# Kernel optimization log

Measured on AMD Instinct MI355X. Metric: run time of the kernel, lower is better.

Reference implementation:

```python
import jax, jax.numpy as jnp
import numpy as np
import math

B, S, H, NH = 2, 2048, 2048, 16
HD = H // NH
BASE = 10000.0


def _rope_tables():
    inv_freq = 1.0 / (BASE ** (np.arange(0, HD, 2, dtype=np.float32) / HD))
    t = np.arange(S, dtype=np.float32)
    freqs = np.einsum('i,j->ij', t, inv_freq)          # [S, HD/2]
    emb = np.concatenate([freqs, freqs], axis=-1)       # [S, HD]
    return jnp.asarray(np.cos(emb)), jnp.asarray(np.sin(emb))


def setup_inputs() -> dict:
    key = jax.random.key(0)
    ks = jax.random.split(key, 6)
    scale = 1.0 / math.sqrt(H)
    cos, sin = _rope_tables()
    causal = np.triu(np.full((S, S), -1e9, dtype=np.float32), k=1)
    attn_bias = jnp.broadcast_to(jnp.asarray(causal)[None, None], (B, 1, S, S))
    return {
        'hidden_states': jax.random.normal(ks[0], (B, S, H), jnp.float32),
        'masks': jnp.zeros((B, S, S), jnp.float32),
        'attn_bias': attn_bias,
        'cos': cos,
        'sin': sin,
        'wq': jax.random.normal(ks[1], (H, H), jnp.float32) * scale,
        'wk': jax.random.normal(ks[2], (H, H), jnp.float32) * scale,
        'wv': jax.random.normal(ks[3], (H, H), jnp.float32) * scale,
        'wo': jax.random.normal(ks[4], (H, H), jnp.float32) * scale,
        'position_ids': jnp.broadcast_to(jnp.arange(S, dtype=jnp.int64)[None], (B, S)),
    }


def _rotate_half(x):
    x1, x2 = x[..., : x.shape[-1] // 2], x[..., x.shape[-1] // 2:]
    return jnp.concatenate([-x2, x1], axis=-1)


def reference(hidden_states, masks, attn_bias, cos, sin, wq, wk, wv, wo, position_ids):
    b, s, h = hidden_states.shape
    nh, hd = NH, HD
    # QKV projections (torch Linear: x @ W.T), split heads -> [b, nh, s, hd]
    def proj(w):
        return (hidden_states @ w.T).reshape(b, s, nh, hd).transpose(0, 2, 1, 3)
    q, k, v = proj(wq), proj(wk), proj(wv)
    # RoPE
    cos_p = cos[position_ids][:, None]  # [b, 1, s, hd]
    sin_p = sin[position_ids][:, None]
    q = q * cos_p + _rotate_half(q) * sin_p
    k = k * cos_p + _rotate_half(k) * sin_p
    # attention scores with additive masks (mx_attn branch, fp math)
    att = jnp.einsum('bhqd,bhkd->bhqk', q / math.sqrt(hd), k)
    att = att + attn_bias + masks[:, None]
    att = jax.nn.softmax(att, axis=-1)
    out = jnp.einsum('bhqk,bhkd->bhqd', att, v)
    out = out.transpose(0, 2, 1, 3).reshape(b, s, h)
    return out @ wo.T
```

## Files before the change

### kernel.cpp

```cpp
#include <hip/hip_runtime.h>
#include <stdint.h>

#define B_  2
#define S_  2048
#define H_  2048
#define NH_ 16
#define HD_ 128

typedef __bf16 v8bf __attribute__((ext_vector_type(8)));
typedef float  v4f  __attribute__((ext_vector_type(4)));

__device__ __forceinline__ float b2f(unsigned short u) {
  union { unsigned int i; float f; } x; x.i = ((unsigned int)u) << 16; return x.f;
}
__device__ __forceinline__ unsigned short f2b(float f) {
  union { float f; unsigned int i; } x; x.f = f;
  unsigned int r = x.i + 0x7FFFu + ((x.i >> 16) & 1u);
  return (unsigned short)(r >> 16);
}

__device__ __forceinline__ void async16(const void* g, void* l) {
  __builtin_amdgcn_global_load_lds(
      (const __attribute__((address_space(1))) void*)g,
      (__attribute__((address_space(3))) void*)l, 16, 0, 0);
}

__global__ __launch_bounds__(256) void cvt_all(const float* __restrict__ hid,
                                               const float* __restrict__ wq,
                                               const float* __restrict__ wk,
                                               const float* __restrict__ wv,
                                               const float* __restrict__ wo,
                                               unsigned short* __restrict__ Xb,
                                               unsigned short* __restrict__ Wqb,
                                               unsigned short* __restrict__ Wkb,
                                               unsigned short* __restrict__ Wvb,
                                               unsigned short* __restrict__ Wob) {
  int bid = blockIdx.x;
  const float* src;
  unsigned short* dst;
  int rel;
  if (bid < 8192)       { src = hid; dst = Xb;  rel = bid; }
  else if (bid < 12288) { src = wq;  dst = Wqb; rel = bid - 8192; }
  else if (bid < 16384) { src = wk;  dst = Wkb; rel = bid - 12288; }
  else if (bid < 20480) { src = wv;  dst = Wvb; rel = bid - 16384; }
  else                  { src = wo;  dst = Wob; rel = bid - 20480; }
  int i = rel * 256 + threadIdx.x;
  float4 f = *(const float4*)(src + (size_t)i * 4);
  ushort4 u;
  u.x = f2b(f.x); u.y = f2b(f.y); u.z = f2b(f.z); u.w = f2b(f.w);
  *(ushort4*)(dst + (size_t)i * 4) = u;
}

__device__ __forceinline__ void gemm_tile_nt(const unsigned short* __restrict__ A,
                                             const unsigned short* __restrict__ Bm,
                                             int m0, int n0, int Kdim,
                                             unsigned short* As, unsigned short* Bs,
                                             v4f (&acc)[2][8]) {
  const int tid = threadIdx.x;
  const int lane = tid & 63, w = tid >> 6;
  const int lr = lane & 15, lg = lane >> 4;
  const int wm = w * 32;

  for (int k0 = 0; k0 < Kdim; k0 += 32) {
    __syncthreads();
#pragma unroll
    for (int i = 0; i < 2; ++i) {
      const int cbase = i * 256 + w * 64;
      const int cc = cbase + lane;
      const int row = cc >> 2, col = (cc & 3) << 3;
      async16(A  + (size_t)(m0 + row) * Kdim + k0 + col, (char*)As + (size_t)cbase * 16);
      async16(Bm + (size_t)(n0 + row) * Kdim + k0 + col, (char*)Bs + (size_t)cbase * 16);
    }
    __syncthreads();
    v8bf a[2], bb[8];
#pragma unroll
    for (int i = 0; i < 2; i++) a[i]  = *(const v8bf*)(As + (wm + i * 16 + lr) * 32 + lg * 8);
#pragma unroll
    for (int i = 0; i < 8; i++) bb[i] = *(const v8bf*)(Bs + (i * 16 + lr) * 32 + lg * 8);
#pragma unroll
    for (int mi = 0; mi < 2; mi++)
#pragma unroll
      for (int ni = 0; ni < 8; ni++)
        acc[mi][ni] = __builtin_amdgcn_mfma_f32_16x16x32_bf16(a[mi], bb[ni], acc[mi][ni], 0, 0, 0);
  }
}

__global__ __launch_bounds__(512, 2) void gemm_qkv(const unsigned short* __restrict__ X,
                                                   const unsigned short* __restrict__ Wq,
                                                   const unsigned short* __restrict__ Wk,
                                                   const unsigned short* __restrict__ Wv,
                                                   const float* __restrict__ cosT,
                                                   const float* __restrict__ sinT,
                                                   unsigned short* __restrict__ Qo,
                                                   unsigned short* __restrict__ Ko,
                                                   unsigned short* __restrict__ Vt) {
  __shared__ __align__(16) unsigned short lds[4][256 * 64];

  const int tid = threadIdx.x, lane = tid & 63, w = tid >> 6;
  const int lr = lane & 15, lg = lane >> 4;
  const int m0 = blockIdx.x * 256;
  const int by = blockIdx.y;
  const int xsw = (lr & 7) << 3;

  auto stgA = [&](const unsigned short* G, int g0, int k0, unsigned short* dst) {
#pragma unroll
    for (int i = 0; i < 4; ++i) {
      const int cbase = i * 512 + w * 64;
      const int cc = cbase + lane;
      const int row = cc >> 3;
      const int kq = (cc & 7) ^ (row & 7);
      async16(G + (size_t)(g0 + row) * H_ + k0 + kq * 8, (char*)dst + (size_t)cbase * 16);
    }
  };
  auto stgB128 = [&](const unsigned short* G, int g0, int k0, unsigned short* dst) {
#pragma unroll
    for (int i = 0; i < 2; ++i) {
      const int cbase = i * 512 + w * 64;
      const int cc = cbase + lane;
      const int row = cc >> 3;
      const int kq = (cc & 7) ^ (row & 7);
      async16(G + (size_t)(g0 + row) * H_ + k0 + kq * 8, (char*)dst + (size_t)cbase * 16);
    }
  };

  {
    const int nq = by & 7;
    const int n0 = nq * 256;
    const unsigned short* Bw = (by < 8) ? Wq : Wk;
    const int wm = w >> 1, wn = w & 1;

    v4f acc[4][8];
#pragma unroll
    for (int i = 0; i < 4; i++)
#pragma unroll
      for (int j = 0; j < 8; j++) { v4f z = {0.f, 0.f, 0.f, 0.f}; acc[i][j] = z; }

    stgA(X,  m0, 0, lds[0]);
    stgA(Bw, n0, 0, lds[1]);
    __syncthreads();

    for (int t = 0; t < 32; ++t) {
      const unsigned short* As = lds[(t & 1) * 2];
      const unsigned short* Bs = lds[(t & 1) * 2 + 1];
      unsigned short* Ad = lds[((t + 1) & 1) * 2];
      unsigned short* Bd = lds[((t + 1) & 1) * 2 + 1];
      const int kn = (t + 1) * 64;
      v8bf bf[8][2], af[2];

      if (t < 31) stgA(X, m0, kn, Ad);
#pragma unroll
      for (int ni = 0; ni < 8; ni++) {
        const unsigned short* rp = Bs + (size_t)(wn * 128 + ni * 16 + lr) * 64;
        bf[ni][0] = *(const v8bf*)(rp + ((lg * 8) ^ xsw));
        bf[ni][1] = *(const v8bf*)(rp + ((32 + lg * 8) ^ xsw));
      }
      {
        const unsigned short* rp = As + (size_t)(wm * 64 + lr) * 64;
        af[0] = *(const v8bf*)(rp + ((lg * 8) ^ xsw));
        af[1] = *(const v8bf*)(rp + ((32 + lg * 8) ^ xsw));
      }
      __builtin_amdgcn_s_barrier();
      asm volatile("s_waitcnt lgkmcnt(0)" ::: "memory");
      __builtin_amdgcn_sched_barrier(0);
      __builtin_amdgcn_s_setprio(1);
#pragma unroll
      for (int ni = 0; ni < 8; ni++) {
        acc[0][ni] = __builtin_amdgcn_mfma_f32_16x16x32_bf16(af[0], bf[ni][0], acc[0][ni], 0, 0, 0);
        acc[0][ni] = __builtin_amdgcn_mfma_f32_16x16x32_bf16(af[1], bf[ni][1], acc[0][ni], 0, 0, 0);
      }
      __builtin_amdgcn_s_setprio(0);
      __builtin_amdgcn_s_barrier();

      if (t < 31) stgA(Bw, n0, kn, Bd);
      {
        const unsigned short* rp = As + (size_t)(wm * 64 + 16 + lr) * 64;
        af[0] = *(const v8bf*)(rp + ((lg * 8) ^ xsw));
        af[1] = *(const v8bf*)(rp + ((32 + lg * 8) ^ xsw));
      }
      __builtin_amdgcn_s_barrier();
      asm volatile("s_waitcnt lgkmcnt(0)" ::: "memory");
      __builtin_amdgcn_sched_barrier(0);
      __builtin_amdgcn_s_setprio(1);
#pragma unroll
      for (int ni = 0; ni < 8; ni++) {
        acc[1][ni] = __builtin_amdgcn_mfma_f32_16x16x32_bf16(af[0], bf[ni][0], acc[1][ni], 0, 0, 0);
        acc[1][ni] = __builtin_amdgcn_mfma_f32_16x16x32_bf16(af[1], bf[ni][1], acc[1][ni], 0, 0, 0);
      }
      __builtin_amdgcn_s_setprio(0);
      __builtin_amdgcn_s_barrier();

      {
        const unsigned short* rp = As + (size_t)(wm * 64 + 32 + lr) * 64;
        af[0] = *(const v8bf*)(rp + ((lg * 8) ^ xsw));
        af[1] = *(const v8bf*)(rp + ((32 + lg * 8) ^ xsw));
      }
      __builtin_amdgcn_s_barrier();
      asm volatile("s_waitcnt lgkmcnt(0)" ::: "memory");
      __builtin_amdgcn_sched_barrier(0);
      __builtin_amdgcn_s_setprio(1);
#pragma unroll
      for (int ni = 0; ni < 8; ni++) {
        acc[2][ni] = __builtin_amdgcn_mfma_f32_16x16x32_bf16(af[0], bf[ni][0], acc[2][ni], 0, 0, 0);
        acc[2][ni] = __builtin_amdgcn_mfma_f32_16x16x32_bf16(af[1], bf[ni][1], acc[2][ni], 0, 0, 0);
      }
      __builtin_amdgcn_s_setprio(0);
      __builtin_amdgcn_s_barrier();

      {
        const unsigned short* rp = As + (size_t)(wm * 64 + 48 + lr) * 64;
        af[0] = *(const v8bf*)(rp + ((lg * 8) ^ xsw));
        af[1] = *(const v8bf*)(rp + ((32 + lg * 8) ^ xsw));
      }
      __builtin_amdgcn_s_barrier();
      asm volatile("s_waitcnt lgkmcnt(0)" ::: "memory");
      __builtin_amdgcn_sched_barrier(0);
      __builtin_amdgcn_s_setprio(1);
#pragma unroll
      for (int ni = 0; ni < 8; ni++) {
        acc[3][ni] = __builtin_amdgcn_mfma_f32_16x16x32_bf16(af[0], bf[ni][0], acc[3][ni], 0, 0, 0);
        acc[3][ni] = __builtin_amdgcn_mfma_f32_16x16x32_bf16(af[1], bf[ni][1], acc[3][ni], 0, 0, 0);
      }
      __builtin_amdgcn_s_setprio(0);
      __syncthreads();
    }

    const int h = nq * 2 + wn;
    const int rb0 = m0 + wm * 64;
    unsigned short* Out = (by < 8) ? Qo : Ko;
    const float sc = (by < 8) ? (float)(0.08838834764831845 * 1.4426950408889634) : 1.0f;
#pragma unroll
    for (int mi = 0; mi < 4; mi++)
#pragma unroll
      for (int ni = 0; ni < 4; ni++)
#pragma unroll
        for (int r = 0; r < 4; r++) {
          int row = rb0 + mi * 16 + lg * 4 + r;
          int s = row & 2047;
          int d = ni * 16 + lr;
          float c  = cosT[(size_t)s * HD_ + d];
          float sn = sinT[(size_t)s * HD_ + d];
          float x1 = acc[mi][ni][r], x2 = acc[mi][ni + 4][r];
          Out[(size_t)row * H_ + h * HD_ + d]      = f2b((x1 * c - x2 * sn) * sc);
          Out[(size_t)row * H_ + h * HD_ + d + 64] = f2b((x2 * c + x1 * sn) * sc);
        }
  }

  {
    const int n0v = by * 128;
    const int wm = w >> 1, wn = w & 1;

    v4f acc[4][4];
#pragma unroll
    for (int i = 0; i < 4; i++)
#pragma unroll
      for (int j = 0; j < 4; j++) { v4f z = {0.f, 0.f, 0.f, 0.f}; acc[i][j] = z; }

    stgA(X, m0, 0, lds[0]);
    stgB128(Wv, n0v, 0, lds[1]);
    __syncthreads();

    for (int t = 0; t < 32; ++t) {
      const unsigned short* As = lds[(t & 1) * 2];
      const unsigned short* Bs = lds[(t & 1) * 2 + 1];
      unsigned short* Ad = lds[((t + 1) & 1) * 2];
      unsigned short* Bd = lds[((t + 1) & 1) * 2 + 1];
      const int kn = (t + 1) * 64;
      v8bf bf[4][2], af[2];

      if (t < 31) stgA(X, m0, kn, Ad);
#pragma unroll
      for (int ni = 0; ni < 4; ni++) {
        const unsigned short* rp = Bs + (size_t)(wn * 64 + ni * 16 + lr) * 64;
        bf[ni][0] = *(const v8bf*)(rp + ((lg * 8) ^ xsw));
        bf[ni][1] = *(const v8bf*)(rp + ((32 + lg * 8) ^ xsw));
      }
      {
        const unsigned short* rp = As + (size_t)(wm * 64 + lr) * 64;
        af[0] = *(const v8bf*)(rp + ((lg * 8) ^ xsw));
        af[1] = *(const v8bf*)(rp + ((32 + lg * 8) ^ xsw));
      }
      __builtin_amdgcn_s_barrier();
      asm volatile("s_waitcnt lgkmcnt(0)" ::: "memory");
      __builtin_amdgcn_sched_barrier(0);
      __builtin_amdgcn_s_setprio(1);
#pragma unroll
      for (int ni = 0; ni < 4; ni++) {
        acc[0][ni] = __builtin_amdgcn_mfma_f32_16x16x32_bf16(af[0], bf[ni][0], acc[0][ni], 0, 0, 0);
        acc[0][ni] = __builtin_amdgcn_mfma_f32_16x16x32_bf16(af[1], bf[ni][1], acc[0][ni], 0, 0, 0);
      }
      __builtin_amdgcn_s_setprio(0);
      __builtin_amdgcn_s_barrier();

      if (t < 31) stgB128(Wv, n0v, kn, Bd);
      {
        const unsigned short* rp = As + (size_t)(wm * 64 + 16 + lr) * 64;
        af[0] = *(const v8bf*)(rp + ((lg * 8) ^ xsw));
        af[1] = *(const v8bf*)(rp + ((32 + lg * 8) ^ xsw));
      }
      __builtin_amdgcn_s_barrier();
      asm volatile("s_waitcnt lgkmcnt(0)" ::: "memory");
      __builtin_amdgcn_sched_barrier(0);
      __builtin_amdgcn_s_setprio(1);
#pragma unroll
      for (int ni = 0; ni < 4; ni++) {
        acc[1][ni] = __builtin_amdgcn_mfma_f32_16x16x32_bf16(af[0], bf[ni][0], acc[1][ni], 0, 0, 0);
        acc[1][ni] = __builtin_amdgcn_mfma_f32_16x16x32_bf16(af[1], bf[ni][1], acc[1][ni], 0, 0, 0);
      }
      __builtin_amdgcn_s_setprio(0);
      __builtin_amdgcn_s_barrier();

      {
        const unsigned short* rp = As + (size_t)(wm * 64 + 32 + lr) * 64;
        af[0] = *(const v8bf*)(rp + ((lg * 8) ^ xsw));
        af[1] = *(const v8bf*)(rp + ((32 + lg * 8) ^ xsw));
      }
      __builtin_amdgcn_s_barrier();
      asm volatile("s_waitcnt lgkmcnt(0)" ::: "memory");
      __builtin_amdgcn_sched_barrier(0);
      __builtin_amdgcn_s_setprio(1);
#pragma unroll
      for (int ni = 0; ni < 4; ni++) {
        acc[2][ni] = __builtin_amdgcn_mfma_f32_16x16x32_bf16(af[0], bf[ni][0], acc[2][ni], 0, 0, 0);
        acc[2][ni] = __builtin_amdgcn_mfma_f32_16x16x32_bf16(af[1], bf[ni][1], acc[2][ni], 0, 0, 0);
      }
      __builtin_amdgcn_s_setprio(0);
      __builtin_amdgcn_s_barrier();

      {
        const unsigned short* rp = As + (size_t)(wm * 64 + 48 + lr) * 64;
        af[0] = *(const v8bf*)(rp + ((lg * 8) ^ xsw));
        af[1] = *(const v8bf*)(rp + ((32 + lg * 8) ^ xsw));
      }
      __builtin_amdgcn_s_barrier();
      asm volatile("s_waitcnt lgkmcnt(0)" ::: "memory");
      __builtin_amdgcn_sched_barrier(0);
      __builtin_amdgcn_s_setprio(1);
#pragma unroll
      for (int ni = 0; ni < 4; ni++) {
        acc[3][ni] = __builtin_amdgcn_mfma_f32_16x16x32_bf16(af[0], bf[ni][0], acc[3][ni], 0, 0, 0);
        acc[3][ni] = __builtin_amdgcn_mfma_f32_16x16x32_bf16(af[1], bf[ni][1], acc[3][ni], 0, 0, 0);
      }
      __builtin_amdgcn_s_setprio(0);
      __syncthreads();
    }

    const int h = by;
#pragma unroll
    for (int mi = 0; mi < 4; mi++)
#pragma unroll
      for (int ni = 0; ni < 4; ni++) {
        int row0 = m0 + wm * 64 + mi * 16 + lg * 4;
        int b = row0 >> 11, s0 = row0 & 2047;
        int d = wn * 64 + ni * 16 + lr;
        ushort4 u;
        u.x = f2b(acc[mi][ni][0]); u.y = f2b(acc[mi][ni][1]);
        u.z = f2b(acc[mi][ni][2]); u.w = f2b(acc[mi][ni][3]);
        *(ushort4*)(Vt + ((size_t)((b * NH_ + h) * HD_) + d) * S_ + s0) = u;
      }
  }
}

__global__ __launch_bounds__(256, 2) void gemm_out(const unsigned short* __restrict__ A,
                                                   const unsigned short* __restrict__ Wo,
                                                   float* __restrict__ Out) {
  __shared__ unsigned short As[128 * 32], Bs[128 * 32];
  const int m0 = blockIdx.x * 128;
  const int n0 = blockIdx.y * 128;

  v4f acc[2][8];
#pragma unroll
  for (int i = 0; i < 2; i++)
#pragma unroll
    for (int j = 0; j < 8; j++) { v4f z = {0.f, 0.f, 0.f, 0.f}; acc[i][j] = z; }

  gemm_tile_nt(A, Wo, m0, n0, H_, As, Bs, acc);

  const int lane = threadIdx.x & 63, w = threadIdx.x >> 6;
  const int lr = lane & 15, lg = lane >> 4;
#pragma unroll
  for (int mi = 0; mi < 2; mi++)
#pragma unroll
    for (int ni = 0; ni < 8; ni++)
#pragma unroll
      for (int r = 0; r < 4; r++)
        Out[(size_t)(m0 + w * 32 + mi * 16 + lg * 4 + r) * H_ + n0 + ni * 16 + lr] =
            acc[mi][ni][r];
}

#define KT_ 64

__global__ __launch_bounds__(512, 2) void attn_kernel(const unsigned short* __restrict__ Qb,
                                                      const unsigned short* __restrict__ Kb,
                                                      const unsigned short* __restrict__ Vt,
                                                      unsigned short* __restrict__ Ob) {
  __shared__ __align__(16) char smem[90112];
  unsigned short* Ps = (unsigned short*)(smem + 71680);

  const int tid = threadIdx.x, lane = tid & 63, w = tid >> 6;
  const int lr = lane & 15, lg = lane >> 4;
  const int qp = blockIdx.x, h = blockIdx.y, b = blockIdx.z;

  const int wtile = (w < 4) ? qp : (15 - qp);
  const int wrow = wtile * 128 + (w & 3) * 32;
  const int nkt = (16 - qp) * 2;

  auto stage = [&](int kt, char* Kd) {
    const int k0 = kt * KT_;
    char* Vd = Kd + 17408;
#pragma unroll
    for (int i = 0; i < 3; ++i) {
      int cbase = i * 512 + w * 64;
      if (cbase < 1088) {
        int cc = cbase + lane;
        int row = cc / 17, pos = cc % 17;
        int p2 = (pos == 16) ? 0 : pos;
        async16(Kb + (size_t)(b * S_ + k0 + row) * H_ + h * HD_ + p2 * 8,
                Kd + (size_t)cbase * 16);
      }
    }
#pragma unroll
    for (int i = 0; i < 3; ++i) {
      int cbase = i * 512 + w * 64;
      if (cbase < 1152) {
        int cc = cbase + lane;
        int row = cc / 9, pos = cc % 9;
        int p2 = (pos == 8) ? 0 : pos;
        async16(Vt + ((size_t)((b * NH_ + h) * HD_ + row)) * S_ + k0 + p2 * 8,
                Vd + (size_t)cbase * 16);
      }
    }
  };

  v8bf qf[2][4];
#pragma unroll
  for (int mt = 0; mt < 2; mt++)
#pragma unroll
    for (int ks = 0; ks < 4; ks++)
      qf[mt][ks] = *(const v8bf*)(Qb + (size_t)(b * S_ + wrow + mt * 16 + lr) * H_ +
                                  h * HD_ + ks * 32 + lg * 8);

  v4f o[2][8];
#pragma unroll
  for (int mt = 0; mt < 2; mt++)
#pragma unroll
    for (int nt = 0; nt < 8; nt++) { v4f z = {0.f, 0.f, 0.f, 0.f}; o[mt][nt] = z; }
  float mst[2][4], lst[2][4];
#pragma unroll
  for (int mt = 0; mt < 2; mt++)
#pragma unroll
    for (int r = 0; r < 4; r++) { mst[mt][r] = -1e30f; lst[mt][r] = 0.f; }

  stage(0, smem);
  __syncthreads();

  int cur = 0;
  for (int kt = 0; kt < nkt; kt++) {
    char* curb = smem + cur * 35840;
    if (kt + 1 < nkt) stage(kt + 1, smem + (cur ^ 1) * 35840);

    unsigned short* Ks = (unsigned short*)curb;
    unsigned short* Vs = (unsigned short*)(curb + 17408);
    const int k0 = kt * KT_;

    if (k0 <= wrow + 31) {
      v4f sacc[2][4];
#pragma unroll
      for (int mt = 0; mt < 2; mt++)
#pragma unroll
        for (int nt = 0; nt < 4; nt++) { v4f z = {0.f, 0.f, 0.f, 0.f}; sacc[mt][nt] = z; }
#pragma unroll
      for (int nt = 0; nt < 4; nt++) {
        v8bf kf[4];
#pragma unroll
        for (int ks = 0; ks < 4; ks++)
          kf[ks] = *(const v8bf*)(Ks + (nt * 16 + lr) * 136 + ks * 32 + lg * 8);
#pragma unroll
        for (int mt = 0; mt < 2; mt++)
#pragma unroll
          for (int ks = 0; ks < 4; ks++)
            sacc[mt][nt] =
                __builtin_amdgcn_mfma_f32_16x16x32_bf16(qf[mt][ks], kf[ks], sacc[mt][nt], 0, 0, 0);
      }
      if (k0 + KT_ - 1 > wrow) {
#pragma unroll
        for (int mt = 0; mt < 2; mt++)
#pragma unroll
          for (int nt = 0; nt < 4; nt++)
#pragma unroll
            for (int r = 0; r < 4; r++) {
              int key = k0 + nt * 16 + lr;
              int query = wrow + mt * 16 + lg * 4 + r;
              if (key > query) sacc[mt][nt][r] = -1e30f;
            }
      }
#pragma unroll
      for (int mt = 0; mt < 2; mt++) {
        float rmax[4], alpha[4], rsum[4];
#pragma unroll
        for (int r = 0; r < 4; r++) {
          float v = fmaxf(fmaxf(sacc[mt][0][r], sacc[mt][1][r]),
                          fmaxf(sacc[mt][2][r], sacc[mt][3][r]));
#pragma unroll
          for (int off = 8; off >= 1; off >>= 1) v = fmaxf(v, __shfl_xor(v, off, 64));
          rmax[r] = v;
        }
#pragma unroll
        for (int r = 0; r < 4; r++) {
          float mnew = fmaxf(mst[mt][r], rmax[r]);
          alpha[r] = exp2f(mst[mt][r] - mnew);
          mst[mt][r] = mnew;
          rsum[r] = 0.f;
        }
#pragma unroll
        for (int nt = 0; nt < 4; nt++)
#pragma unroll
          for (int r = 0; r < 4; r++) {
            float p = exp2f(sacc[mt][nt][r] - mst[mt][r]);
            sacc[mt][nt][r] = p;
            rsum[r] += p;
          }
#pragma unroll
        for (int r = 0; r < 4; r++) {
#pragma unroll
          for (int off = 8; off >= 1; off >>= 1) rsum[r] += __shfl_xor(rsum[r], off, 64);
          lst[mt][r] = lst[mt][r] * alpha[r] + rsum[r];
        }
#pragma unroll
        for (int nt = 0; nt < 8; nt++)
#pragma unroll
          for (int r = 0; r < 4; r++) o[mt][nt][r] *= alpha[r];
      }
      v8bf bv[8][2];
#pragma unroll
      for (int nt = 0; nt < 8; nt++)
#pragma unroll
        for (int ks = 0; ks < 2; ks++)
          bv[nt][ks] = *(const v8bf*)(Vs + (nt * 16 + lr) * 72 + ks * 32 + lg * 8);
#pragma unroll
      for (int mt = 0; mt < 2; mt++) {
#pragma unroll
        for (int nt = 0; nt < 4; nt++)
#pragma unroll
          for (int r = 0; r < 4; r++) {
            union { float f; unsigned u; } pu; pu.f = sacc[mt][nt][r];
            Ps[w * 1152 + (lg * 4 + r) * 72 + nt * 16 + lr] =
                (unsigned short)(pu.u >> 16);
          }
        asm volatile("" ::: "memory");
        v8bf af[2];
#pragma unroll
        for (int ks = 0; ks < 2; ks++)
          af[ks] = *(const v8bf*)(Ps + w * 1152 + lr * 72 + ks * 32 + lg * 8);
#pragma unroll
        for (int nt = 0; nt < 8; nt++)
#pragma unroll
          for (int ks = 0; ks < 2; ks++)
            o[mt][nt] = __builtin_amdgcn_mfma_f32_16x16x32_bf16(af[ks], bv[nt][ks], o[mt][nt], 0, 0, 0);
        asm volatile("" ::: "memory");
      }
    }
    __syncthreads();
    cur ^= 1;
  }
#pragma unroll
  for (int mt = 0; mt < 2; mt++) {
    float inv[4];
#pragma unroll
    for (int r = 0; r < 4; r++) inv[r] = 1.f / lst[mt][r];
#pragma unroll
    for (int nt = 0; nt < 8; nt++)
#pragma unroll
      for (int r = 0; r < 4; r++) {
        int row = wrow + mt * 16 + lg * 4 + r;
        int col = h * HD_ + nt * 16 + lr;
        Ob[(size_t)(b * S_ + row) * H_ + col] = f2b(o[mt][nt][r] * inv[r]);
      }
  }
}

extern "C" void kernel_launch(void* const* d_in, const int* in_sizes, int n_in,
                              void* d_out, int out_size, void* d_ws, size_t ws_size,
                              hipStream_t stream) {
  const float* hidden = (const float*)d_in[0];
  const float* cosT = (const float*)d_in[3];
  const float* sinT = (const float*)d_in[4];
  const float* wq = (const float*)d_in[5];
  const float* wk = (const float*)d_in[6];
  const float* wv = (const float*)d_in[7];
  const float* wo = (const float*)d_in[8];
  float* out = (float*)d_out;

  char* p = (char*)d_ws;
  const size_t SZ_X = (size_t)4096 * 2048 * 2;
  const size_t SZ_W = (size_t)2048 * 2048 * 2;
  unsigned short* Xb  = (unsigned short*)p; p += SZ_X;
  unsigned short* Wqb = (unsigned short*)p; p += SZ_W;
  unsigned short* Wkb = (unsigned short*)p; p += SZ_W;
  unsigned short* Wvb = (unsigned short*)p; p += SZ_W;
  unsigned short* Wob = (unsigned short*)p; p += SZ_W;
  unsigned short* Qb  = (unsigned short*)p; p += SZ_X;
  unsigned short* Kb  = (unsigned short*)p; p += SZ_X;
  unsigned short* Vt  = (unsigned short*)p; p += SZ_X;
  unsigned short* Ob  = (unsigned short*)p; p += SZ_X;

  cvt_all<<<24576, 256, 0, stream>>>(hidden, wq, wk, wv, wo, Xb, Wqb, Wkb, Wvb, Wob);
  gemm_qkv<<<dim3(16, 16), 512, 0, stream>>>(Xb, Wqb, Wkb, Wvb, cosT, sinT, Qb, Kb, Vt);
  attn_kernel<<<dim3(8, 16, 2), 512, 0, stream>>>(Qb, Kb, Vt, Ob);
  gemm_out<<<dim3(32, 16), 256, 0, stream>>>(Ob, Wob, out);
}
```

Baseline: 434.3 us.

## Rebalance causal attention work per wave and swizzle K/V shared-memory layout

Each of the 8 waves now owns 16 rows from the long query tile and 16 rows from its mirrored short tile, rather than waves 0-3 taking one tile and 4-7 the other. This balances causal work across waves, and MFMA and softmax for the short tile are skipped once it is fully masked. K/V LDS tiles drop padding in favour of an XOR swizzle, shrinking shared memory, and row reductions use ds_swizzle instead of shfl_xor. The per-wave branch on act1 adds divergence-free predication but more code paths.

```diff
diff --git a/kernel.cpp b/kernel.cpp
--- a/kernel.cpp
+++ b/kernel.cpp
@@ -23,6 +23,21 @@
   __builtin_amdgcn_global_load_lds(
       (const __attribute__((address_space(1))) void*)g,
       (__attribute__((address_space(3))) void*)l, 16, 0, 0);
+}
+
+__device__ __forceinline__ float swz_max16(float v) {
+  v = fmaxf(v, __int_as_float(__builtin_amdgcn_ds_swizzle(__float_as_int(v), 0x201F)));
+  v = fmaxf(v, __int_as_float(__builtin_amdgcn_ds_swizzle(__float_as_int(v), 0x101F)));
+  v = fmaxf(v, __int_as_float(__builtin_amdgcn_ds_swizzle(__float_as_int(v), 0x081F)));
+  v = fmaxf(v, __int_as_float(__builtin_amdgcn_ds_swizzle(__float_as_int(v), 0x041F)));
+  return v;
+}
+__device__ __forceinline__ float swz_sum16(float v) {
+  v += __int_as_float(__builtin_amdgcn_ds_swizzle(__float_as_int(v), 0x201F));
+  v += __int_as_float(__builtin_amdgcn_ds_swizzle(__float_as_int(v), 0x101F));
+  v += __int_as_float(__builtin_amdgcn_ds_swizzle(__float_as_int(v), 0x081F));
+  v += __int_as_float(__builtin_amdgcn_ds_swizzle(__float_as_int(v), 0x041F));
+  return v;
 }
 
 __global__ __launch_bounds__(256) void cvt_all(const float* __restrict__ hid,
@@ -393,51 +408,47 @@
                                                       const unsigned short* __restrict__ Kb,
                                                       const unsigned short* __restrict__ Vt,
                                                       unsigned short* __restrict__ Ob) {
-  __shared__ __align__(16) char smem[90112];
-  unsigned short* Ps = (unsigned short*)(smem + 71680);
+  __shared__ __align__(16) char smem[83968];
+  unsigned short* Ps = (unsigned short*)(smem + 65536);
 
   const int tid = threadIdx.x, lane = tid & 63, w = tid >> 6;
   const int lr = lane & 15, lg = lane >> 4;
   const int qp = blockIdx.x, h = blockIdx.y, b = blockIdx.z;
 
-  const int wtile = (w < 4) ? qp : (15 - qp);
-  const int wrow = wtile * 128 + (w & 3) * 32;
+  const int lrow = (15 - qp) * 128 + w * 16;
+  const int srow = qp * 128 + w * 16;
   const int nkt = (16 - qp) * 2;
+  const int xsw = (lr & 7) << 3;
 
   auto stage = [&](int kt, char* Kd) {
     const int k0 = kt * KT_;
-    char* Vd = Kd + 17408;
-#pragma unroll
-    for (int i = 0; i < 3; ++i) {
+    char* Vd = Kd + 16384;
+#pragma unroll
+    for (int i = 0; i < 2; ++i) {
       int cbase = i * 512 + w * 64;
-      if (cbase < 1088) {
-        int cc = cbase + lane;
-        int row = cc / 17, pos = cc % 17;
-        int p2 = (pos == 16) ? 0 : pos;
-        async16(Kb + (size_t)(b * S_ + k0 + row) * H_ + h * HD_ + p2 * 8,
-                Kd + (size_t)cbase * 16);
-      }
-    }
-#pragma unroll
-    for (int i = 0; i < 3; ++i) {
+      int cc = cbase + lane;
+      int row = cc >> 4, pos = cc & 15;
+      async16(Kb + (size_t)(b * S_ + k0 + row) * H_ + h * HD_ + ((pos ^ (row & 7)) << 3),
+              Kd + (size_t)cbase * 16);
+    }
+#pragma unroll
+    for (int i = 0; i < 2; ++i) {
       int cbase = i * 512 + w * 64;
-      if (cbase < 1152) {
-        int cc = cbase + lane;
-        int row = cc / 9, pos = cc % 9;
-        int p2 = (pos == 8) ? 0 : pos;
-        async16(Vt + ((size_t)((b * NH_ + h) * HD_ + row)) * S_ + k0 + p2 * 8,
-                Vd + (size_t)cbase * 16);
-      }
+      int cc = cbase + lane;
+      int row = cc >> 3, pos = cc & 7;
+      async16(Vt + ((size_t)((b * NH_ + h) * HD_ + row)) * S_ + k0 + ((pos ^ (row & 7)) << 3),
+              Vd + (size_t)cbase * 16);
     }
   };
 
   v8bf qf[2][4];
 #pragma unroll
-  for (int mt = 0; mt < 2; mt++)
-#pragma unroll
-    for (int ks = 0; ks < 4; ks++)
-      qf[mt][ks] = *(const v8bf*)(Qb + (size_t)(b * S_ + wrow + mt * 16 + lr) * H_ +
-                                  h * HD_ + ks * 32 + lg * 8);
+  for (int ks = 0; ks < 4; ks++) {
+    qf[0][ks] = *(const v8bf*)(Qb + (size_t)(b * S_ + lrow + lr) * H_ +
+                               h * HD_ + ks * 32 + lg * 8);
+    qf[1][ks] = *(const v8bf*)(Qb + (size_t)(b * S_ + srow + lr) * H_ +
+                               h * HD_ + ks * 32 + lg * 8);
+  }
 
   v4f o[2][8];
 #pragma unroll
@@ -455,14 +466,15 @@
 
   int cur = 0;
   for (int kt = 0; kt < nkt; kt++) {
-    char* curb = smem + cur * 35840;
-    if (kt + 1 < nkt) stage(kt + 1, smem + (cur ^ 1) * 35840);
+    char* curb = smem + cur * 32768;
+    if (kt + 1 < nkt) stage(kt + 1, smem + (cur ^ 1) * 32768);
 
     unsigned short* Ks = (unsigned short*)curb;
-    unsigned short* Vs = (unsigned short*)(curb + 17408);
+    unsigned short* Vs = (unsigned short*)(curb + 16384);
     const int k0 = kt * KT_;
 
-    if (k0 <= wrow + 31) {
+    if (k0 <= lrow + 15) {
+      const bool act1 = (k0 <= srow + 15);
       v4f sacc[2][4];
 #pragma unroll
       for (int mt = 0; mt < 2; mt++)
@@ -473,40 +485,43 @@
         v8bf kf[4];
 #pragma unroll
         for (int ks = 0; ks < 4; ks++)
-          kf[ks] = *(const v8bf*)(Ks + (nt * 16 + lr) * 136 + ks * 32 + lg * 8);
-#pragma unroll
-        for (int mt = 0; mt < 2; mt++)
+          kf[ks] = *(const v8bf*)(Ks + (nt * 16 + lr) * 128 + ((ks * 32 + lg * 8) ^ xsw));
+#pragma unroll
+        for (int ks = 0; ks < 4; ks++)
+          sacc[0][nt] = __builtin_amdgcn_mfma_f32_16x16x32_bf16(qf[0][ks], kf[ks], sacc[0][nt], 0, 0, 0);
+        if (act1)
 #pragma unroll
           for (int ks = 0; ks < 4; ks++)
-            sacc[mt][nt] =
-                __builtin_amdgcn_mfma_f32_16x16x32_bf16(qf[mt][ks], kf[ks], sacc[mt][nt], 0, 0, 0);
-      }
-      if (k0 + KT_ - 1 > wrow) {
-#pragma unroll
-        for (int mt = 0; mt < 2; mt++)
-#pragma unroll
-          for (int nt = 0; nt < 4; nt++)
-#pragma unroll
-            for (int r = 0; r < 4; r++) {
-              int key = k0 + nt * 16 + lr;
-              int query = wrow + mt * 16 + lg * 4 + r;
-              if (key > query) sacc[mt][nt][r] = -1e30f;
-            }
+            sacc[1][nt] = __builtin_amdgcn_mfma_f32_16x16x32_bf16(qf[1][ks], kf[ks], sacc[1][nt], 0, 0, 0);
+      }
+      if (k0 + 63 > lrow) {
+#pragma unroll
+        for (int nt = 0; nt < 4; nt++)
+#pragma unroll
+          for (int r = 0; r < 4; r++) {
+            int key = k0 + nt * 16 + lr;
+            if (key > lrow + lg * 4 + r) sacc[0][nt][r] = -1e30f;
+          }
+      }
+      if (act1 && k0 + 63 > srow) {
+#pragma unroll
+        for (int nt = 0; nt < 4; nt++)
+#pragma unroll
+          for (int r = 0; r < 4; r++) {
+            int key = k0 + nt * 16 + lr;
+            if (key > srow + lg * 4 + r) sacc[1][nt][r] = -1e30f;
+          }
       }
 #pragma unroll
       for (int mt = 0; mt < 2; mt++) {
-        float rmax[4], alpha[4], rsum[4];
+        if (mt == 1 && !act1) continue;
+        float alpha[4], rsum[4];
 #pragma unroll
         for (int r = 0; r < 4; r++) {
           float v = fmaxf(fmaxf(sacc[mt][0][r], sacc[mt][1][r]),
                           fmaxf(sacc[mt][2][r], sacc[mt][3][r]));
-#pragma unroll
-          for (int off = 8; off >= 1; off >>= 1) v = fmaxf(v, __shfl_xor(v, off, 64));
-          rmax[r] = v;
-        }
-#pragma unroll
-        for (int r = 0; r < 4; r++) {
-          float mnew = fmaxf(mst[mt][r], rmax[r]);
+          v = swz_max16(v);
+          float mnew = fmaxf(mst[mt][r], v);
           alpha[r] = exp2f(mst[mt][r] - mnew);
           mst[mt][r] = mnew;
           rsum[r] = 0.f;
@@ -521,8 +536,7 @@
           }
 #pragma unroll
         for (int r = 0; r < 4; r++) {
-#pragma unroll
-          for (int off = 8; off >= 1; off >>= 1) rsum[r] += __shfl_xor(rsum[r], off, 64);
+          rsum[r] = swz_sum16(rsum[r]);
           lst[mt][r] = lst[mt][r] * alpha[r] + rsum[r];
         }
 #pragma unroll
@@ -535,9 +549,10 @@
       for (int nt = 0; nt < 8; nt++)
 #pragma unroll
         for (int ks = 0; ks < 2; ks++)
-          bv[nt][ks] = *(const v8bf*)(Vs + (nt * 16 + lr) * 72 + ks * 32 + lg * 8);
+          bv[nt][ks] = *(const v8bf*)(Vs + (nt * 16 + lr) * 64 + ((ks * 32 + lg * 8) ^ xsw));
 #pragma unroll
       for (int mt = 0; mt < 2; mt++) {
+        if (mt == 1 && !act1) continue;
 #pragma unroll
         for (int nt = 0; nt < 4; nt++)
 #pragma unroll
@@ -564,6 +579,7 @@
   }
 #pragma unroll
   for (int mt = 0; mt < 2; mt++) {
+    const int rbase = (mt == 0) ? lrow : srow;
     float inv[4];
 #pragma unroll
     for (int r = 0; r < 4; r++) inv[r] = 1.f / lst[mt][r];
@@ -571,7 +587,7 @@
     for (int nt = 0; nt < 8; nt++)
 #pragma unroll
       for (int r = 0; r < 4; r++) {
-        int row = wrow + mt * 16 + lg * 4 + r;
+        int row = rbase + lg * 4 + r;
         int col = h * HD_ + nt * 16 + lr;
         Ob[(size_t)(b * S_ + row) * H_ + col] = f2b(o[mt][nt][r] * inv[r]);
       }
```

After: 402.7 us. 1.08x faster.
